# Kernel optimization log

Hardware: AMD Instinct MI355X
Metric: run time of the kernel (lower is better)

## Reference

```python
import jax, jax.numpy as jnp
import numpy as np

B, S, IN, D, H, L, F = 4, 1024, 6, 512, 8, 4, 2048
DK = D // H
EPS = 1e-5

def _pos_encoding(S, D):
    pos = np.arange(S, dtype=np.float32)[:, None]
    div = np.exp(np.arange(0, D, 2, dtype=np.float32) * (-np.log(10000.0) / D))
    pe = np.zeros((S, D), np.float32)
    pe[:, 0::2] = np.sin(pos * div)
    pe[:, 1::2] = np.cos(pos * div)
    return jnp.asarray(pe)

def setup_inputs() -> dict:
    key = jax.random.key(0)
    ks = jax.random.split(key, 12)
    def w(k, shape):
        return jax.random.normal(k, shape, jnp.float32) * 0.02
    return {
        "left_wrist": jax.random.normal(ks[0], (B, S, IN), jnp.float32),
        "right_wrist": jax.random.normal(ks[1], (B, S, IN), jnp.float32),
        "Wl": w(ks[2], (IN, D)), "bl": jnp.zeros((D,), jnp.float32),
        "Wr": w(ks[3], (IN, D)), "br": jnp.zeros((D,), jnp.float32),
        "pe": _pos_encoding(S, D),
        # 4 attention blocks per layer (cross1to2, cross2to1, self1, self2), each with q/k/v/o projections
        "mha_w": w(ks[4], (L, 4, 4, D, D)), "mha_b": jnp.zeros((L, 4, 4, D), jnp.float32),
        "mha_ln_g": jnp.ones((L, 4, D), jnp.float32), "mha_ln_b": jnp.zeros((L, 4, D), jnp.float32),
        # 2 FFNs per layer (channel 1 / channel 2)
        "ff_w1": w(ks[5], (L, 2, D, F)), "ff_b1": jnp.zeros((L, 2, F), jnp.float32),
        "ff_w2": w(ks[6], (L, 2, F, D)), "ff_b2": jnp.zeros((L, 2, D), jnp.float32),
        "ff_ln_g": jnp.ones((L, 2, D), jnp.float32), "ff_ln_b": jnp.zeros((L, 2, D), jnp.float32),
        "h1_w1": w(ks[7], (2 * D, D)), "h1_b1": jnp.zeros((D,), jnp.float32),
        "h1_w2": w(ks[8], (D, 2)), "h1_b2": jnp.zeros((2,), jnp.float32),
        "h2_w1": w(ks[9], (2 * D, D)), "h2_b1": jnp.zeros((D,), jnp.float32),
        "h2_w2": w(ks[10], (D, 2)), "h2_b2": jnp.zeros((2,), jnp.float32),
    }

def _ln(x, g, b):
    m = jnp.mean(x, axis=-1, keepdims=True)
    v = jnp.var(x, axis=-1, keepdims=True)
    return (x - m) * jax.lax.rsqrt(v + EPS) * g + b

def _mha(q_in, k_in, v_in, w, b, g, beta):
    # w: [4, D, D] for q/k/v/o, b: [4, D]
    def proj(x, i):
        return (x @ w[i] + b[i]).reshape(x.shape[0], x.shape[1], H, DK).transpose(0, 2, 1, 3)
    Q, K, V = proj(q_in, 0), proj(k_in, 1), proj(v_in, 2)
    scores = jnp.einsum('bhqd,bhkd->bhqk', Q, K) * np.float32(1.0 / np.sqrt(DK))
    attn = jax.nn.softmax(scores, axis=-1)
    ctx = jnp.einsum('bhqk,bhkd->bhqd', attn, V)
    ctx = ctx.transpose(0, 2, 1, 3).reshape(q_in.shape[0], q_in.shape[1], D)
    out = ctx @ w[3] + b[3]
    return _ln(out + q_in, g, beta)

def _ffn(x, w1, b1, w2, b2, g, beta):
    h = jax.nn.relu(x @ w1 + b1)
    return _ln(h @ w2 + b2 + x, g, beta)

def reference(left_wrist, right_wrist, Wl, bl, Wr, br, pe,
              mha_w, mha_b, mha_ln_g, mha_ln_b,
              ff_w1, ff_b1, ff_w2, ff_b2, ff_ln_g, ff_ln_b,
              h1_w1, h1_b1, h1_w2, h1_b2, h2_w1, h2_b1, h2_w2, h2_b2):
    left = left_wrist @ Wl + bl + pe[None]
    right = right_wrist @ Wr + br + pe[None]
    for l in range(L):
        lc = _mha(left, right, right, mha_w[l, 0], mha_b[l, 0], mha_ln_g[l, 0], mha_ln_b[l, 0])
        rc = _mha(right, left, left, mha_w[l, 1], mha_b[l, 1], mha_ln_g[l, 1], mha_ln_b[l, 1])
        ls = _mha(lc, lc, lc, mha_w[l, 2], mha_b[l, 2], mha_ln_g[l, 2], mha_ln_b[l, 2])
        rs = _mha(rc, rc, rc, mha_w[l, 3], mha_b[l, 3], mha_ln_g[l, 3], mha_ln_b[l, 3])
        left = _ffn(ls, ff_w1[l, 0], ff_b1[l, 0], ff_w2[l, 0], ff_b2[l, 0], ff_ln_g[l, 0], ff_ln_b[l, 0])
        right = _ffn(rs, ff_w1[l, 1], ff_b1[l, 1], ff_w2[l, 1], ff_b2[l, 1], ff_ln_g[l, 1], ff_ln_b[l, 1])
    # AdaptiveAvgPool1d(1) over seq == mean over seq axis
    fused = jnp.concatenate([jnp.mean(left, axis=1), jnp.mean(right, axis=1)], axis=1)  # [B, 2D]
    logits1 = jax.nn.relu(fused @ h1_w1 + h1_b1) @ h1_w2 + h1_b2
    logits2 = jax.nn.relu(fused @ h2_w1 + h2_b1) @ h2_w2 + h2_b2
    return (logits1, logits2)
```

## Files before the change

### kernel.cpp

```cpp
#include <hip/hip_runtime.h>
#include <hip/hip_bf16.h>

#define NB 4
#define NS 1024
#define NIN 6
#define ND 512
#define NH 8
#define NLAYERS 4
#define NF 2048
#define NDK 64
#define LN_EPS 1e-5f

typedef unsigned short u16;
typedef __attribute__((ext_vector_type(4))) unsigned short u16x4;
typedef __attribute__((ext_vector_type(8))) short s16x8;
typedef __attribute__((ext_vector_type(4))) float f32x4;
typedef __attribute__((ext_vector_type(4))) unsigned int u32x4;

#define MFMA_BF16(A, B, C) __builtin_amdgcn_mfma_f32_16x16x32_bf16(A, B, C, 0, 0, 0)

#define GLOAD_LDS16(gsrc, ldst)                                                  \
    __builtin_amdgcn_global_load_lds(                                            \
        (const __attribute__((address_space(1))) void*)(gsrc),                   \
        (__attribute__((address_space(3))) void*)(ldst), 16, 0, 0)

__device__ inline u16 f2bf(float f) {
    unsigned int u = __builtin_bit_cast(unsigned int, f);
    u += 0x7fffu + ((u >> 16) & 1u);
    return (u16)(u >> 16);
}

__global__ __launch_bounds__(256) void transpose_kernel(
    const float* __restrict__ src, u16* __restrict__ dst, int K, int N) {
    __shared__ u16 t[64][72];
    const int tid = threadIdx.x;
    src += (size_t)blockIdx.z * K * N;
    dst += (size_t)blockIdx.z * K * N;
    const int n0 = blockIdx.x * 64, k0 = blockIdx.y * 64;
    {
        int r = tid >> 2, cq = (tid & 3) * 16;
        const float* sp = src + (size_t)(k0 + r) * N + n0 + cq;
#pragma unroll
        for (int q = 0; q < 4; ++q) {
            float4 v = *reinterpret_cast<const float4*>(sp + q * 4);
            t[r][cq + q * 4 + 0] = f2bf(v.x);
            t[r][cq + q * 4 + 1] = f2bf(v.y);
            t[r][cq + q * 4 + 2] = f2bf(v.z);
            t[r][cq + q * 4 + 3] = f2bf(v.w);
        }
    }
    __syncthreads();
    {
        int rn = tid >> 2, cq = (tid & 3) * 16;
        s16x8 o0, o1;
#pragma unroll
        for (int j = 0; j < 8; ++j) o0[j] = (short)t[cq + j][rn];
#pragma unroll
        for (int j = 0; j < 8; ++j) o1[j] = (short)t[cq + 8 + j][rn];
        u16* dp = dst + (size_t)(n0 + rn) * K + k0 + cq;
        *reinterpret_cast<s16x8*>(dp) = o0;
        *reinterpret_cast<s16x8*>(dp + 8) = o1;
    }
}

__global__ __launch_bounds__(256) void in_proj_kernel(
    const float* __restrict__ x, const float* __restrict__ W,
    const float* __restrict__ bias, const float* __restrict__ pe,
    float* __restrict__ out, u16* __restrict__ outb) {
    int idx = blockIdx.x * 256 + threadIdx.x;
    int d = idx & (ND - 1);
    int bs = idx / ND;
    int s = bs & (NS - 1);
    const float* xr = x + (size_t)bs * NIN;
    float acc = bias[d] + pe[(size_t)s * ND + d];
#pragma unroll
    for (int i = 0; i < NIN; ++i) acc += xr[i] * W[(size_t)i * ND + d];
    out[idx] = acc;
    outb[idx] = f2bf(acc);
}

template <int BN>
__device__ inline void gemm_core(const u16* __restrict__ A, const u16* __restrict__ Wt,
                                 int K, int bm, int bn, char* lds, int tid,
                                 f32x4 (&acc)[4][BN / 32]) {
    constexpr int NT = BN / 32;
    constexpr int ASZ = 128 * 128;
    constexpr int BSZ = BN * 128;
    const int wid = tid >> 6, lane = tid & 63;
    const int l15 = lane & 15, lhi = lane >> 4;
    const int wr = wid >> 1, wc = wid & 1;

    auto stage = [&](int buf, int k0) {
#pragma unroll
        for (int i = 0; i < 4; ++i) {
            int slot = (wid * 4 + i) * 64 + lane;
            int r = slot >> 3, p = slot & 7;
            const char* src = (const char*)(A + (size_t)(bm + r) * K + k0)
                              + ((p * 16) ^ ((r & 7) << 4));
            GLOAD_LDS16(src, lds + buf * ASZ + (wid * 4 + i) * 1024);
        }
#pragma unroll
        for (int i = 0; i < BN / 32; ++i) {
            int slot = (wid * (BN / 32) + i) * 64 + lane;
            int r = slot >> 3, p = slot & 7;
            const char* src = (const char*)(Wt + (size_t)(bn + r) * K + k0)
                              + ((p * 16) ^ ((r & 7) << 4));
            GLOAD_LDS16(src, lds + 2 * ASZ + buf * BSZ + (wid * (BN / 32) + i) * 1024);
        }
    };

#pragma unroll
    for (int mt = 0; mt < 4; ++mt)
#pragma unroll
        for (int nt = 0; nt < NT; ++nt) acc[mt][nt] = f32x4{0.f, 0.f, 0.f, 0.f};

    const int KT = K >> 6;
    stage(0, 0);
    __syncthreads();
    for (int t = 0; t < KT; ++t) {
        if (t + 1 < KT) stage((t + 1) & 1, (t + 1) << 6);
        const char* Ab = lds + (t & 1) * ASZ;
        const char* Bb = lds + 2 * ASZ + (t & 1) * BSZ;
#pragma unroll
        for (int sl = 0; sl < 2; ++sl) {
            s16x8 af[4];
#pragma unroll
            for (int mt = 0; mt < 4; ++mt) {
                int row = wr * 64 + mt * 16 + l15;
                af[mt] = *reinterpret_cast<const s16x8*>(
                    Ab + ((row * 128 + sl * 64 + lhi * 16) ^ ((row & 7) << 4)));
            }
            s16x8 bfr[NT];
#pragma unroll
            for (int nt = 0; nt < NT; ++nt) {
                int row = wc * (BN / 2) + nt * 16 + l15;
                bfr[nt] = *reinterpret_cast<const s16x8*>(
                    Bb + ((row * 128 + sl * 64 + lhi * 16) ^ ((row & 7) << 4)));
            }
#pragma unroll
            for (int mt = 0; mt < 4; ++mt)
#pragma unroll
                for (int nt = 0; nt < NT; ++nt)
                    acc[mt][nt] = MFMA_BF16(af[mt], bfr[nt], acc[mt][nt]);
        }
        __syncthreads();
    }
}

template <int OMODE, int BN>
__global__ __launch_bounds__(256) void bgemm2_kernel(
    const u16* __restrict__ a0, const u16* __restrict__ a1,
    const u16* __restrict__ wt0, const u16* __restrict__ wt1,
    const float* __restrict__ bias0, const float* __restrict__ bias1,
    void* __restrict__ Cv, int M, int N, int K) {
    constexpr int NT = BN / 32;
    __shared__ char lds[2 * 128 * 128 + 2 * BN * 128];
    const int tid = threadIdx.x, z = blockIdx.z;
    const int bm = blockIdx.y * 128, bn = blockIdx.x * BN;
    const u16* A = z ? a1 : a0;
    const u16* Wt = z ? wt1 : wt0;
    const float* bias = z ? bias1 : bias0;

    f32x4 acc[4][NT];
    gemm_core<BN>(A, Wt, K, bm, bn, lds, tid, acc);

    const int wid = tid >> 6, lane = tid & 63;
    const int l15 = lane & 15, lhi = lane >> 4;
    const int wr = wid >> 1, wc = wid & 1;
    float bv[NT];
#pragma unroll
    for (int nt = 0; nt < NT; ++nt) bv[nt] = bias[bn + wc * (BN / 2) + nt * 16 + l15];

    if (OMODE == 0) {
        float* C = (float*)Cv + (size_t)z * M * N;
#pragma unroll
        for (int mt = 0; mt < 4; ++mt) {
            int m0 = bm + wr * 64 + mt * 16 + lhi * 4;
#pragma unroll
            for (int nt = 0; nt < NT; ++nt) {
                int n = bn + wc * (BN / 2) + nt * 16 + l15;
#pragma unroll
                for (int r = 0; r < 4; ++r)
                    C[(size_t)(m0 + r) * N + n] = acc[mt][nt][r] + bv[nt];
            }
        }
    } else {
        u16* C = (u16*)Cv + (size_t)z * M * N;
#pragma unroll
        for (int mt = 0; mt < 4; ++mt) {
            int m0 = bm + wr * 64 + mt * 16 + lhi * 4;
#pragma unroll
            for (int nt = 0; nt < NT; ++nt) {
                int n = bn + wc * (BN / 2) + nt * 16 + l15;
#pragma unroll
                for (int r = 0; r < 4; ++r) {
                    float v = acc[mt][nt][r] + bv[nt];
                    if (OMODE == 1) v = fmaxf(v, 0.f);
                    C[(size_t)(m0 + r) * N + n] = f2bf(v);
                }
            }
        }
    }
}

__global__ __launch_bounds__(256) void bgemm_qkv_kernel(
    const u16* __restrict__ aq0, const u16* __restrict__ aq1,
    const u16* __restrict__ akv0, const u16* __restrict__ akv1,
    const u16* __restrict__ wt0, const u16* __restrict__ wt1,
    const float* __restrict__ bb0, const float* __restrict__ bb1,
    u16* __restrict__ Qo, u16* __restrict__ Ko, u16* __restrict__ Vto) {
    __shared__ char lds[2 * 128 * 128 + 2 * 64 * 128];
    const int tid = threadIdx.x, z = blockIdx.z;
    const int proj = blockIdx.x >> 3;
    const int bm = blockIdx.y * 128, bn = (blockIdx.x & 7) * 64;
    const int M = NB * NS;
    const u16* A = (proj == 0) ? (z ? aq1 : aq0) : (z ? akv1 : akv0);
    const u16* Wt = (z ? wt1 : wt0) + (size_t)proj * ND * ND;
    const float* bias = (z ? bb1 : bb0) + proj * ND;

    f32x4 acc[4][2];
    gemm_core<64>(A, Wt, ND, bm, bn, lds, tid, acc);

    const int wid = tid >> 6, lane = tid & 63;
    const int l15 = lane & 15, lhi = lane >> 4;
    const int wr = wid >> 1, wc = wid & 1;
    float bv[2];
#pragma unroll
    for (int nt = 0; nt < 2; ++nt) bv[nt] = bias[bn + wc * 32 + nt * 16 + l15];

    if (proj < 2) {
        u16* C = (proj ? Ko : Qo) + (size_t)z * M * ND;
#pragma unroll
        for (int mt = 0; mt < 4; ++mt) {
            int m0 = bm + wr * 64 + mt * 16 + lhi * 4;
#pragma unroll
            for (int nt = 0; nt < 2; ++nt) {
                int n = bn + wc * 32 + nt * 16 + l15;
#pragma unroll
                for (int r = 0; r < 4; ++r)
                    C[(size_t)(m0 + r) * ND + n] = f2bf(acc[mt][nt][r] + bv[nt]);
            }
        }
    } else {
#pragma unroll
        for (int mt = 0; mt < 4; ++mt) {
            int m0 = bm + wr * 64 + mt * 16 + lhi * 4;
            int b = (z * M + m0) >> 10, s = m0 & (NS - 1);
#pragma unroll
            for (int nt = 0; nt < 2; ++nt) {
                int n = bn + wc * 32 + nt * 16 + l15;
                int h = n >> 6, dk = n & 63;
                u16x4 o = {f2bf(acc[mt][nt][0] + bv[nt]), f2bf(acc[mt][nt][1] + bv[nt]),
                           f2bf(acc[mt][nt][2] + bv[nt]), f2bf(acc[mt][nt][3] + bv[nt])};
                *reinterpret_cast<u16x4*>(Vto + ((size_t)((b * NH + h) * NDK + dk)) * NS + s) = o;
            }
        }
    }
}

__global__ __launch_bounds__(256) void ln2_kernel(
    const float* __restrict__ x, const float* __restrict__ res,
    const float* __restrict__ g0, const float* __restrict__ g1,
    const float* __restrict__ be0, const float* __restrict__ be1,
    float* __restrict__ outf, u16* __restrict__ outb) {
    int row = blockIdx.x;
    const float* g = (row >> 12) ? g1 : g0;
    const float* be = (row >> 12) ? be1 : be0;
    int tid = threadIdx.x;
    const float* xr = x + (size_t)row * ND;
    const float* rr = res + (size_t)row * ND;
    float v0 = xr[tid] + rr[tid];
    float v1 = xr[tid + 256] + rr[tid + 256];
    float s = v0 + v1, sq = v0 * v0 + v1 * v1;
#pragma unroll
    for (int m = 1; m < 64; m <<= 1) { s += __shfl_xor(s, m); sq += __shfl_xor(sq, m); }
    __shared__ float ls[4], lq[4];
    int wid = tid >> 6, lane = tid & 63;
    if (lane == 0) { ls[wid] = s; lq[wid] = sq; }
    __syncthreads();
    s = ls[0] + ls[1] + ls[2] + ls[3];
    sq = lq[0] + lq[1] + lq[2] + lq[3];
    float mean = s * (1.f / ND);
    float var = sq * (1.f / ND) - mean * mean;
    float rstd = rsqrtf(var + LN_EPS);
    float o0 = (v0 - mean) * rstd * g[tid] + be[tid];
    float o1 = (v1 - mean) * rstd * g[tid + 256] + be[tid + 256];
    outf[(size_t)row * ND + tid] = o0;
    outf[(size_t)row * ND + tid + 256] = o1;
    outb[(size_t)row * ND + tid] = f2bf(o0);
    outb[(size_t)row * ND + tid + 256] = f2bf(o1);
}

__global__ __launch_bounds__(256) void attn_kernel(
    const u16* __restrict__ Qb, const u16* __restrict__ Kb,
    const u16* __restrict__ Vtb, u16* __restrict__ O) {
    __shared__ u16 Ks[128 * 64];
    __shared__ u16 Vts[64 * 128];
    __shared__ u16 Ps[4][16 * 128];

    const int tid = threadIdx.x;
    const int w = tid >> 6, lane = tid & 63;
    const int l15 = lane & 15, lhi = lane >> 4;
    const int bh = blockIdx.y;
    const int b = bh >> 3, h = bh & 7;
    const int qb = blockIdx.x * 64 + w * 16;

    s16x8 qf[2];
    {
        const u16* qp = Qb + ((size_t)(b * NS) + qb + l15) * ND + h * NDK + lhi * 8;
        qf[0] = *reinterpret_cast<const s16x8*>(qp);
        qf[1] = *reinterpret_cast<const s16x8*>(qp + 32);
    }

    f32x4 o[4] = {f32x4{0.f, 0.f, 0.f, 0.f}, f32x4{0.f, 0.f, 0.f, 0.f},
                  f32x4{0.f, 0.f, 0.f, 0.f}, f32x4{0.f, 0.f, 0.f, 0.f}};
    float m = -1e30f;
    float lsum = 0.f;

    const u16* Kbase = Kb + ((size_t)(b * NS)) * ND + h * NDK;
    const u16* Vbase = Vtb + ((size_t)bh * NDK) * NS;

    for (int c = 0; c < NS / 128; ++c) {
        const int kv0 = c * 128;
        __syncthreads();
#pragma unroll
        for (int i = 0; i < 4; ++i) {
            int s = i * 256 + tid;
            {
                int r = s >> 3, p = s & 7;
                u32x4 kv = *reinterpret_cast<const u32x4*>(
                    Kbase + (size_t)(kv0 + r) * ND + p * 8);
                *reinterpret_cast<u32x4*>((char*)Ks +
                    ((r * 128 + p * 16) ^ ((r & 7) << 4))) = kv;
            }
            {
                int r = s >> 4, p = s & 15;
                u32x4 vv = *reinterpret_cast<const u32x4*>(
                    Vbase + (size_t)r * NS + kv0 + p * 8);
                *reinterpret_cast<u32x4*>((char*)Vts +
                    ((r * 256 + p * 16) ^ ((r & 7) << 4))) = vv;
            }
        }
        __syncthreads();

        f32x4 sc[8];
#pragma unroll
        for (int blk = 0; blk < 8; ++blk) sc[blk] = f32x4{0.f, 0.f, 0.f, 0.f};
#pragma unroll
        for (int sl = 0; sl < 2; ++sl) {
#pragma unroll
            for (int blk = 0; blk < 8; ++blk) {
                int krow = blk * 16 + l15;
                s16x8 kf = *reinterpret_cast<const s16x8*>((char*)Ks +
                    ((krow * 128 + sl * 64 + lhi * 16) ^ ((krow & 7) << 4)));
                sc[blk] = MFMA_BF16(kf, qf[sl], sc[blk]);
            }
        }
        float mx = -1e30f;
#pragma unroll
        for (int blk = 0; blk < 8; ++blk) {
#pragma unroll
            for (int r = 0; r < 4; ++r) {
                float v = sc[blk][r] * 0.125f;
                sc[blk][r] = v;
                mx = fmaxf(mx, v);
            }
        }
        mx = fmaxf(mx, __shfl_xor(mx, 16));
        mx = fmaxf(mx, __shfl_xor(mx, 32));
        float mn = fmaxf(m, mx);
        float corr = __expf(m - mn);
        m = mn;
        float rs = 0.f;
#pragma unroll
        for (int blk = 0; blk < 8; ++blk) {
#pragma unroll
            for (int r = 0; r < 4; ++r) {
                float p = __expf(sc[blk][r] - mn);
                sc[blk][r] = p;
                rs += p;
            }
        }
        rs += __shfl_xor(rs, 16);
        rs += __shfl_xor(rs, 32);
        lsum = lsum * corr + rs;
#pragma unroll
        for (int blk = 0; blk < 8; ++blk) {
            u16x4 pk = {f2bf(sc[blk][0]), f2bf(sc[blk][1]),
                        f2bf(sc[blk][2]), f2bf(sc[blk][3])};
            *reinterpret_cast<u16x4*>((char*)(Ps[w]) +
                ((l15 * 256 + blk * 32 + lhi * 8) ^ ((l15 & 7) << 4))) = pk;
        }
        float cO[4];
#pragma unroll
        for (int r = 0; r < 4; ++r) cO[r] = __shfl(corr, lhi * 4 + r);
#pragma unroll
        for (int db = 0; db < 4; ++db)
#pragma unroll
            for (int r = 0; r < 4; ++r) o[db][r] *= cO[r];
#pragma unroll
        for (int sl2 = 0; sl2 < 4; ++sl2) {
            s16x8 pf = *reinterpret_cast<const s16x8*>((char*)(Ps[w]) +
                ((l15 * 256 + sl2 * 64 + lhi * 16) ^ ((l15 & 7) << 4)));
#pragma unroll
            for (int db = 0; db < 4; ++db) {
                int vr = db * 16 + l15;
                s16x8 vf = *reinterpret_cast<const s16x8*>((char*)Vts +
                    ((vr * 256 + sl2 * 64 + lhi * 16) ^ ((vr & 7) << 4)));
                o[db] = MFMA_BF16(pf, vf, o[db]);
            }
        }
    }
    float lsO[4];
#pragma unroll
    for (int r = 0; r < 4; ++r) lsO[r] = __shfl(lsum, lhi * 4 + r);
#pragma unroll
    for (int db = 0; db < 4; ++db) {
#pragma unroll
        for (int r = 0; r < 4; ++r) {
            int q = qb + lhi * 4 + r;
            O[((size_t)(b * NS) + q) * ND + h * NDK + db * 16 + l15] =
                f2bf(o[db][r] / lsO[r]);
        }
    }
}

__global__ __launch_bounds__(256) void pool2_kernel(
    const float* __restrict__ RES, float* __restrict__ fused) {
    const int b = blockIdx.x, half = blockIdx.y, sc = blockIdx.z;
    const size_t NTOK = (size_t)NB * NS * ND;
    const float* src = RES + (half ? NTOK : 0) + ((size_t)(b * NS + sc * 128)) * ND;
    const int tid = threadIdx.x;
#pragma unroll
    for (int cc = 0; cc < 2; ++cc) {
        int c = cc * 256 + tid;
        float s = 0.f;
        for (int r = 0; r < 128; ++r) s += src[(size_t)r * ND + c];
        atomicAdd(&fused[b * 1024 + half * 512 + c], s * (1.f / NS));
    }
}

__global__ __launch_bounds__(256) void head_hidden_kernel(
    const float* __restrict__ fused,
    const float* __restrict__ w1a, const float* __restrict__ b1a,
    const float* __restrict__ w1b, const float* __restrict__ b1b,
    float* __restrict__ hid) {
    const int b = blockIdx.x >> 1, head = blockIdx.x & 1;
    const float* w1 = head ? w1b : w1a;
    const float* b1 = head ? b1b : b1a;
    const int tid = threadIdx.x;
    const int j = blockIdx.y * 64 + (tid & 63);
    const int kq = tid >> 6;
    const float* fr = fused + (size_t)b * (2 * ND);
    float p = 0.f;
    for (int k = kq * 256; k < kq * 256 + 256; ++k)
        p += fr[k] * w1[(size_t)k * ND + j];
    __shared__ float part[4][64];
    part[kq][tid & 63] = p;
    __syncthreads();
    if (tid < 64) {
        float v = part[0][tid] + part[1][tid] + part[2][tid] + part[3][tid] + b1[j];
        hid[(size_t)blockIdx.x * ND + j] = fmaxf(v, 0.f);
    }
}

__global__ __launch_bounds__(256) void head_out_kernel(
    const float* __restrict__ hid,
    const float* __restrict__ w2a, const float* __restrict__ b2a,
    const float* __restrict__ w2b, const float* __restrict__ b2b,
    float* __restrict__ out) {
    const int b = blockIdx.x >> 1, head = blockIdx.x & 1;
    const float* w2 = head ? w2b : w2a;
    const float* b2 = head ? b2b : b2a;
    const int tid = threadIdx.x;
    const float* hr = hid + (size_t)blockIdx.x * ND;
    float h0 = hr[tid], h1 = hr[tid + 256];
    float p0 = h0 * w2[tid * 2 + 0] + h1 * w2[(tid + 256) * 2 + 0];
    float p1 = h0 * w2[tid * 2 + 1] + h1 * w2[(tid + 256) * 2 + 1];
#pragma unroll
    for (int m = 1; m < 64; m <<= 1) { p0 += __shfl_xor(p0, m); p1 += __shfl_xor(p1, m); }
    __shared__ float r0s[4], r1s[4];
    int wid = tid >> 6, lane = tid & 63;
    if (lane == 0) { r0s[wid] = p0; r1s[wid] = p1; }
    __syncthreads();
    if (tid == 0) {
        out[head * 8 + b * 2 + 0] = r0s[0] + r0s[1] + r0s[2] + r0s[3] + b2[0];
        out[head * 8 + b * 2 + 1] = r1s[0] + r1s[1] + r1s[2] + r1s[3] + b2[1];
    }
}

extern "C" void kernel_launch(void* const* d_in, const int* in_sizes, int n_in,
                              void* d_out, int out_size, void* d_ws, size_t ws_size,
                              hipStream_t stream) {
    const float* left_wrist  = (const float*)d_in[0];
    const float* right_wrist = (const float*)d_in[1];
    const float* Wl = (const float*)d_in[2];
    const float* bl = (const float*)d_in[3];
    const float* Wr = (const float*)d_in[4];
    const float* br = (const float*)d_in[5];
    const float* pe = (const float*)d_in[6];
    const float* mha_w    = (const float*)d_in[7];
    const float* mha_b    = (const float*)d_in[8];
    const float* mha_ln_g = (const float*)d_in[9];
    const float* mha_ln_b = (const float*)d_in[10];
    const float* ff_w1 = (const float*)d_in[11];
    const float* ff_b1 = (const float*)d_in[12];
    const float* ff_w2 = (const float*)d_in[13];
    const float* ff_b2 = (const float*)d_in[14];
    const float* ff_ln_g = (const float*)d_in[15];
    const float* ff_ln_b = (const float*)d_in[16];
    const float* h1_w1 = (const float*)d_in[17];
    const float* h1_b1 = (const float*)d_in[18];
    const float* h1_w2 = (const float*)d_in[19];
    const float* h1_b2 = (const float*)d_in[20];
    const float* h2_w1 = (const float*)d_in[21];
    const float* h2_b1 = (const float*)d_in[22];
    const float* h2_w2 = (const float*)d_in[23];
    const float* h2_b2 = (const float*)d_in[24];
    float* out = (float*)d_out;

    const size_t NTOK = (size_t)NB * NS * ND;
    const int M = NB * NS;
    float* ws = (float*)d_ws;
    float* RES   = ws;
    float* CRES  = RES + 2 * NTOK;
    float* TMPf  = CRES + 2 * NTOK;
    float* FUSED = TMPf + 2 * NTOK;
    float* HID   = FUSED + NB * 2 * ND;
    u16* Xbf  = (u16*)(HID + 8 * ND);
    u16* CXbf = Xbf + 2 * NTOK;
    u16* Qbf  = CXbf + 2 * NTOK;
    u16* Kbf  = Qbf + 2 * NTOK;
    u16* Vtbf = Kbf + 2 * NTOK;
    u16* CTbf = Vtbf + 2 * NTOK;
    u16* Hh   = Qbf;
    u16* WtM  = CTbf + 2 * NTOK;
    u16* WtF1 = WtM + (size_t)64 * ND * ND;
    u16* WtF2 = WtF1 + (size_t)8 * ND * NF;

    const size_t DD = (size_t)ND * ND;

    transpose_kernel<<<dim3(ND / 64, ND / 64, 64), 256, 0, stream>>>(mha_w, WtM, ND, ND);
    transpose_kernel<<<dim3(NF / 64, ND / 64, 8), 256, 0, stream>>>(ff_w1, WtF1, ND, NF);
    transpose_kernel<<<dim3(ND / 64, NF / 64, 8), 256, 0, stream>>>(ff_w2, WtF2, NF, ND);

    in_proj_kernel<<<(NB * NS * ND) / 256, 256, 0, stream>>>(left_wrist, Wl, bl, pe, RES, Xbf);
    in_proj_kernel<<<(NB * NS * ND) / 256, 256, 0, stream>>>(right_wrist, Wr, br, pe,
                                                             RES + NTOK, Xbf + NTOK);

    for (int l = 0; l < NLAYERS; ++l) {
        const u16* wt0 = WtM + ((size_t)l * 4 + 0) * 4 * DD;
        const u16* wt1 = WtM + ((size_t)l * 4 + 1) * 4 * DD;
        const u16* wt2 = WtM + ((size_t)l * 4 + 2) * 4 * DD;
        const u16* wt3 = WtM + ((size_t)l * 4 + 3) * 4 * DD;
        const float* bb0 = mha_b + ((size_t)l * 4 + 0) * 4 * ND;
        const float* bb1 = mha_b + ((size_t)l * 4 + 1) * 4 * ND;
        const float* bb2 = mha_b + ((size_t)l * 4 + 2) * 4 * ND;
        const float* bb3 = mha_b + ((size_t)l * 4 + 3) * 4 * ND;

        bgemm_qkv_kernel<<<dim3(24, 32, 2), 256, 0, stream>>>(
            Xbf, Xbf + NTOK, Xbf + NTOK, Xbf, wt0, wt1, bb0, bb1, Qbf, Kbf, Vtbf);
        attn_kernel<<<dim3(NS / 64, 2 * NB * NH), 256, 0, stream>>>(Qbf, Kbf, Vtbf, CTbf);
        bgemm2_kernel<0, 64><<<dim3(8, 32, 2), 256, 0, stream>>>(
            CTbf, CTbf + NTOK, wt0 + 3 * DD, wt1 + 3 * DD, bb0 + 3 * ND, bb1 + 3 * ND,
            TMPf, M, ND, ND);
        ln2_kernel<<<2 * M, 256, 0, stream>>>(
            TMPf, RES, mha_ln_g + ((size_t)l * 4 + 0) * ND, mha_ln_g + ((size_t)l * 4 + 1) * ND,
            mha_ln_b + ((size_t)l * 4 + 0) * ND, mha_ln_b + ((size_t)l * 4 + 1) * ND,
            CRES, CXbf);

        bgemm_qkv_kernel<<<dim3(24, 32, 2), 256, 0, stream>>>(
            CXbf, CXbf + NTOK, CXbf, CXbf + NTOK, wt2, wt3, bb2, bb3, Qbf, Kbf, Vtbf);
        attn_kernel<<<dim3(NS / 64, 2 * NB * NH), 256, 0, stream>>>(Qbf, Kbf, Vtbf, CTbf);
        bgemm2_kernel<0, 64><<<dim3(8, 32, 2), 256, 0, stream>>>(
            CTbf, CTbf + NTOK, wt2 + 3 * DD, wt3 + 3 * DD, bb2 + 3 * ND, bb3 + 3 * ND,
            TMPf, M, ND, ND);
        ln2_kernel<<<2 * M, 256, 0, stream>>>(
            TMPf, CRES, mha_ln_g + ((size_t)l * 4 + 2) * ND, mha_ln_g + ((size_t)l * 4 + 3) * ND,
            mha_ln_b + ((size_t)l * 4 + 2) * ND, mha_ln_b + ((size_t)l * 4 + 3) * ND,
            RES, Xbf);

        bgemm2_kernel<1, 128><<<dim3(16, 32, 2), 256, 0, stream>>>(
            Xbf, Xbf + NTOK, WtF1 + ((size_t)l * 2 + 0) * ND * NF, WtF1 + ((size_t)l * 2 + 1) * ND * NF,
            ff_b1 + ((size_t)l * 2 + 0) * NF, ff_b1 + ((size_t)l * 2 + 1) * NF,
            Hh, M, NF, ND);
        bgemm2_kernel<0, 64><<<dim3(8, 32, 2), 256, 0, stream>>>(
            Hh, Hh + (size_t)M * NF, WtF2 + ((size_t)l * 2 + 0) * NF * ND, WtF2 + ((size_t)l * 2 + 1) * NF * ND,
            ff_b2 + ((size_t)l * 2 + 0) * ND, ff_b2 + ((size_t)l * 2 + 1) * ND,
            TMPf, M, ND, NF);
        ln2_kernel<<<2 * M, 256, 0, stream>>>(
            TMPf, RES, ff_ln_g + ((size_t)l * 2 + 0) * ND, ff_ln_g + ((size_t)l * 2 + 1) * ND,
            ff_ln_b + ((size_t)l * 2 + 0) * ND, ff_ln_b + ((size_t)l * 2 + 1) * ND,
            RES, Xbf);
    }

    hipMemsetAsync(FUSED, 0, NB * 2 * ND * sizeof(float), stream);
    pool2_kernel<<<dim3(NB, 2, 8), 256, 0, stream>>>(RES, FUSED);
    head_hidden_kernel<<<dim3(8, 8), 256, 0, stream>>>(FUSED, h1_w1, h1_b1, h2_w1, h2_b1, HID);
    head_out_kernel<<<8, 256, 0, stream>>>(HID, h1_w2, h1_b2, h2_w2, h2_b2, out);
}
```

Baseline: 1.347 ms.

## Store GEMM outputs as bf16, vectorize layernorm, async LDS loads and exp2 softmax

The output-projection and FFN2 GEMMs now write bf16 instead of fp32 into a temporary buffer, and the layernorm kernel reads that bf16 plus the fp32 residual with paired vector loads and writes paired outputs. The attention kernel loads K and V tiles straight into LDS with global_load_lds, using the XOR swizzle applied on the source side. Softmax folds the 1/8 scale into an exp2 with a log2e constant, and f2bf uses the native bf16 conversion. Together these aim to cut global traffic and ALU work in the pre-layernorm residual path and in attention, at the cost of rounding the pre-residual sums to bf16.

After: 1.351 ms. Within noise of the previous version (+0.2%).

```diff
diff --git a/kernel.cpp b/kernel.cpp
--- a/kernel.cpp
+++ b/kernel.cpp
@@ -25,9 +25,12 @@
         (__attribute__((address_space(3))) void*)(ldst), 16, 0, 0)
 
 __device__ inline u16 f2bf(float f) {
-    unsigned int u = __builtin_bit_cast(unsigned int, f);
-    u += 0x7fffu + ((u >> 16) & 1u);
-    return (u16)(u >> 16);
+    __bf16 h = (__bf16)f;
+    return __builtin_bit_cast(u16, h);
+}
+__device__ inline float bf2f(u16 v) {
+    unsigned int u = (unsigned int)v << 16;
+    return __builtin_bit_cast(float, u);
 }
 
 __global__ __launch_bounds__(256) void transpose_kernel(
@@ -152,7 +155,7 @@
     const u16* __restrict__ a0, const u16* __restrict__ a1,
     const u16* __restrict__ wt0, const u16* __restrict__ wt1,
     const float* __restrict__ bias0, const float* __restrict__ bias1,
-    void* __restrict__ Cv, int M, int N, int K) {
+    u16* __restrict__ Cv, int M, int N, int K) {
     constexpr int NT = BN / 32;
     __shared__ char lds[2 * 128 * 128 + 2 * BN * 128];
     const int tid = threadIdx.x, z = blockIdx.z;
@@ -171,33 +174,18 @@
 #pragma unroll
     for (int nt = 0; nt < NT; ++nt) bv[nt] = bias[bn + wc * (BN / 2) + nt * 16 + l15];
 
-    if (OMODE == 0) {
-        float* C = (float*)Cv + (size_t)z * M * N;
-#pragma unroll
-        for (int mt = 0; mt < 4; ++mt) {
-            int m0 = bm + wr * 64 + mt * 16 + lhi * 4;
-#pragma unroll
-            for (int nt = 0; nt < NT; ++nt) {
-                int n = bn + wc * (BN / 2) + nt * 16 + l15;
-#pragma unroll
-                for (int r = 0; r < 4; ++r)
-                    C[(size_t)(m0 + r) * N + n] = acc[mt][nt][r] + bv[nt];
-            }
-        }
-    } else {
-        u16* C = (u16*)Cv + (size_t)z * M * N;
-#pragma unroll
-        for (int mt = 0; mt < 4; ++mt) {
-            int m0 = bm + wr * 64 + mt * 16 + lhi * 4;
-#pragma unroll
-            for (int nt = 0; nt < NT; ++nt) {
-                int n = bn + wc * (BN / 2) + nt * 16 + l15;
-#pragma unroll
-                for (int r = 0; r < 4; ++r) {
-                    float v = acc[mt][nt][r] + bv[nt];
-                    if (OMODE == 1) v = fmaxf(v, 0.f);
-                    C[(size_t)(m0 + r) * N + n] = f2bf(v);
-                }
+    u16* C = Cv + (size_t)z * M * N;
+#pragma unroll
+    for (int mt = 0; mt < 4; ++mt) {
+        int m0 = bm + wr * 64 + mt * 16 + lhi * 4;
+#pragma unroll
+        for (int nt = 0; nt < NT; ++nt) {
+            int n = bn + wc * (BN / 2) + nt * 16 + l15;
+#pragma unroll
+            for (int r = 0; r < 4; ++r) {
+                float v = acc[mt][nt][r] + bv[nt];
+                if (OMODE == 1) v = fmaxf(v, 0.f);
+                C[(size_t)(m0 + r) * N + n] = f2bf(v);
             }
         }
     }
@@ -259,7 +247,7 @@
 }
 
 __global__ __launch_bounds__(256) void ln2_kernel(
-    const float* __restrict__ x, const float* __restrict__ res,
+    const u16* __restrict__ x, const float* __restrict__ res,
     const float* __restrict__ g0, const float* __restrict__ g1,
     const float* __restrict__ be0, const float* __restrict__ be1,
     float* __restrict__ outf, u16* __restrict__ outb) {
@@ -267,10 +255,10 @@
     const float* g = (row >> 12) ? g1 : g0;
     const float* be = (row >> 12) ? be1 : be0;
     int tid = threadIdx.x;
-    const float* xr = x + (size_t)row * ND;
-    const float* rr = res + (size_t)row * ND;
-    float v0 = xr[tid] + rr[tid];
-    float v1 = xr[tid + 256] + rr[tid + 256];
+    unsigned int xp = *reinterpret_cast<const unsigned int*>(x + (size_t)row * ND + tid * 2);
+    float2 rr = *reinterpret_cast<const float2*>(res + (size_t)row * ND + tid * 2);
+    float v0 = bf2f((u16)(xp & 0xffffu)) + rr.x;
+    float v1 = bf2f((u16)(xp >> 16)) + rr.y;
     float s = v0 + v1, sq = v0 * v0 + v1 * v1;
 #pragma unroll
     for (int m = 1; m < 64; m <<= 1) { s += __shfl_xor(s, m); sq += __shfl_xor(sq, m); }
@@ -283,12 +271,14 @@
     float mean = s * (1.f / ND);
     float var = sq * (1.f / ND) - mean * mean;
     float rstd = rsqrtf(var + LN_EPS);
-    float o0 = (v0 - mean) * rstd * g[tid] + be[tid];
-    float o1 = (v1 - mean) * rstd * g[tid + 256] + be[tid + 256];
-    outf[(size_t)row * ND + tid] = o0;
-    outf[(size_t)row * ND + tid + 256] = o1;
-    outb[(size_t)row * ND + tid] = f2bf(o0);
-    outb[(size_t)row * ND + tid + 256] = f2bf(o1);
+    float2 gg = *reinterpret_cast<const float2*>(g + tid * 2);
+    float2 bb = *reinterpret_cast<const float2*>(be + tid * 2);
+    float o0 = (v0 - mean) * rstd * gg.x + bb.x;
+    float o1 = (v1 - mean) * rstd * gg.y + bb.y;
+    float2 of = {o0, o1};
+    *reinterpret_cast<float2*>(outf + (size_t)row * ND + tid * 2) = of;
+    unsigned int ob = (unsigned int)f2bf(o0) | ((unsigned int)f2bf(o1) << 16);
+    *reinterpret_cast<unsigned int*>(outb + (size_t)row * ND + tid * 2) = ob;
 }
 
 __global__ __launch_bounds__(256) void attn_kernel(
@@ -304,6 +294,7 @@
     const int bh = blockIdx.y;
     const int b = bh >> 3, h = bh & 7;
     const int qb = blockIdx.x * 64 + w * 16;
+    const float c1 = 0.18033688011f;
 
     s16x8 qf[2];
     {
@@ -325,20 +316,18 @@
         __syncthreads();
 #pragma unroll
         for (int i = 0; i < 4; ++i) {
-            int s = i * 256 + tid;
+            int slot = (w * 4 + i) * 64 + lane;
             {
-                int r = s >> 3, p = s & 7;
-                u32x4 kv = *reinterpret_cast<const u32x4*>(
-                    Kbase + (size_t)(kv0 + r) * ND + p * 8);
-                *reinterpret_cast<u32x4*>((char*)Ks +
-                    ((r * 128 + p * 16) ^ ((r & 7) << 4))) = kv;
+                int r = slot >> 3, p = slot & 7;
+                const char* src = (const char*)(Kbase + (size_t)(kv0 + r) * ND)
+                                  + ((p ^ (r & 7)) * 16);
+                GLOAD_LDS16(src, (char*)Ks + (w * 4 + i) * 1024);
             }
             {
-                int r = s >> 4, p = s & 15;
-                u32x4 vv = *reinterpret_cast<const u32x4*>(
-                    Vbase + (size_t)r * NS + kv0 + p * 8);
-                *reinterpret_cast<u32x4*>((char*)Vts +
-                    ((r * 256 + p * 16) ^ ((r & 7) << 4))) = vv;
+                int r = slot >> 4, p = slot & 15;
+                const char* src = (const char*)(Vbase + (size_t)r * NS + kv0)
+                                  + ((p ^ (r & 7)) * 16);
+                GLOAD_LDS16(src, (char*)Vts + (w * 4 + i) * 1024);
             }
         }
         __syncthreads();
@@ -358,25 +347,21 @@
         }
         float mx = -1e30f;
 #pragma unroll
-        for (int blk = 0; blk < 8; ++blk) {
-#pragma unroll
-            for (int r = 0; r < 4; ++r) {
-                float v = sc[blk][r] * 0.125f;
-                sc[blk][r] = v;
-                mx = fmaxf(mx, v);
-            }
-        }
+        for (int blk = 0; blk < 8; ++blk)
+#pragma unroll
+            for (int r = 0; r < 4; ++r) mx = fmaxf(mx, sc[blk][r]);
         mx = fmaxf(mx, __shfl_xor(mx, 16));
         mx = fmaxf(mx, __shfl_xor(mx, 32));
         float mn = fmaxf(m, mx);
-        float corr = __expf(m - mn);
+        float corr = exp2f((m - mn) * c1);
         m = mn;
+        float d = mn * c1;
         float rs = 0.f;
 #pragma unroll
         for (int blk = 0; blk < 8; ++blk) {
 #pragma unroll
             for (int r = 0; r < 4; ++r) {
-                float p = __expf(sc[blk][r] - mn);
+                float p = exp2f(fmaf(sc[blk][r], c1, -d));
                 sc[blk][r] = p;
                 rs += p;
             }
@@ -527,6 +512,7 @@
     float* TMPf  = CRES + 2 * NTOK;
     float* FUSED = TMPf + 2 * NTOK;
     float* HID   = FUSED + NB * 2 * ND;
+    u16* TMPbf = (u16*)TMPf;
     u16* Xbf  = (u16*)(HID + 8 * ND);
     u16* CXbf = Xbf + 2 * NTOK;
     u16* Qbf  = CXbf + 2 * NTOK;
@@ -561,22 +547,22 @@
         bgemm_qkv_kernel<<<dim3(24, 32, 2), 256, 0, stream>>>(
             Xbf, Xbf + NTOK, Xbf + NTOK, Xbf, wt0, wt1, bb0, bb1, Qbf, Kbf, Vtbf);
         attn_kernel<<<dim3(NS / 64, 2 * NB * NH), 256, 0, stream>>>(Qbf, Kbf, Vtbf, CTbf);
-        bgemm2_kernel<0, 64><<<dim3(8, 32, 2), 256, 0, stream>>>(
+        bgemm2_kernel<2, 64><<<dim3(8, 32, 2), 256, 0, stream>>>(
             CTbf, CTbf + NTOK, wt0 + 3 * DD, wt1 + 3 * DD, bb0 + 3 * ND, bb1 + 3 * ND,
-            TMPf, M, ND, ND);
+            TMPbf, M, ND, ND);
         ln2_kernel<<<2 * M, 256, 0, stream>>>(
-            TMPf, RES, mha_ln_g + ((size_t)l * 4 + 0) * ND, mha_ln_g + ((size_t)l * 4 + 1) * ND,
+            TMPbf, RES, mha_ln_g + ((size_t)l * 4 + 0) * ND, mha_ln_g + ((size_t)l * 4 + 1) * ND,
             mha_ln_b + ((size_t)l * 4 + 0) * ND, mha_ln_b + ((size_t)l * 4 + 1) * ND,
             CRES, CXbf);
 
         bgemm_qkv_kernel<<<dim3(24, 32, 2), 256, 0, stream>>>(
             CXbf, CXbf + NTOK, CXbf, CXbf + NTOK, wt2, wt3, bb2, bb3, Qbf, Kbf, Vtbf);
         attn_kernel<<<dim3(NS / 64, 2 * NB * NH), 256, 0, stream>>>(Qbf, Kbf, Vtbf, CTbf);
-        bgemm2_kernel<0, 64><<<dim3(8, 32, 2), 256, 0, stream>>>(
+        bgemm2_kernel<2, 64><<<dim3(8, 32, 2), 256, 0, stream>>>(
             CTbf, CTbf + NTOK, wt2 + 3 * DD, wt3 + 3 * DD, bb2 + 3 * ND, bb3 + 3 * ND,
-            TMPf, M, ND, ND);
+            TMPbf, M, ND, ND);
         ln2_kernel<<<2 * M, 256, 0, stream>>>(
-            TMPf, CRES, mha_ln_g + ((size_t)l * 4 + 2) * ND, mha_ln_g + ((size_t)l * 4 + 3) * ND,
+            TMPbf, CRES, mha_ln_g + ((size_t)l * 4 + 2) * ND, mha_ln_g + ((size_t)l * 4 + 3) * ND,
             mha_ln_b + ((size_t)l * 4 + 2) * ND, mha_ln_b + ((size_t)l * 4 + 3) * ND,
             RES, Xbf);
 
@@ -584,12 +570,12 @@
             Xbf, Xbf + NTOK, WtF1 + ((size_t)l * 2 + 0) * ND * NF, WtF1 + ((size_t)l * 2 + 1) * ND * NF,
             ff_b1 + ((size_t)l * 2 + 0) * NF, ff_b1 + ((size_t)l * 2 + 1) * NF,
             Hh, M, NF, ND);
-        bgemm2_kernel<0, 64><<<dim3(8, 32, 2), 256, 0, stream>>>(
+        bgemm2_kernel<2, 64><<<dim3(8, 32, 2), 256, 0, stream>>>(
             Hh, Hh + (size_t)M * NF, WtF2 + ((size_t)l * 2 + 0) * NF * ND, WtF2 + ((size_t)l * 2 + 1) * NF * ND,
             ff_b2 + ((size_t)l * 2 + 0) * ND, ff_b2 + ((size_t)l * 2 + 1) * ND,
-            TMPf, M, ND, NF);
+            TMPbf, M, ND, NF);
         ln2_kernel<<<2 * M, 256, 0, stream>>>(
-            TMPf, RES, ff_ln_g + ((size_t)l * 2 + 0) * ND, ff_ln_g + ((size_t)l * 2 + 1) * ND,
+            TMPbf, RES, ff_ln_g + ((size_t)l * 2 + 0) * ND, ff_ln_g + ((size_t)l * 2 + 1) * ND,
             ff_ln_b + ((size_t)l * 2 + 0) * ND, ff_ln_b + ((size_t)l * 2 + 1) * ND,
             RES, Xbf);
     }
```
